# Kernel tuning notes

Measured on AMD Instinct MI355X. Metric: run time of the kernel, lower is better.

## Reference

```python
import jax, jax.numpy as jnp
import numpy as np

M = 2048                      # image side (self.M)
INPUT_SHAPE = (362, 362)      # default forward arg; only used for pad sizing
N_ANGLES = 32
THETA = np.linspace(0.0, np.pi, N_ANGLES)  # radians, as the source uses np.cos(angle)


def _dct_mat(N):
    # DCT-II with norm='ortho': C[k, n] = s_k * cos(pi*(n+0.5)*k/N)
    n = np.arange(N)
    C = np.cos(np.pi * (n[None, :] + 0.5) * n[:, None] / N)
    scale = np.full((N, 1), np.sqrt(2.0 / N))
    scale[0, 0] = np.sqrt(1.0 / N)
    return jnp.asarray((C * scale).astype(np.float32))


def _pad_width():
    diagonal = np.sqrt(2) * max(INPUT_SHAPE)
    pad = [int(np.ceil(diagonal - s)) for s in INPUT_SHAPE]
    new_center = [(s + p) // 2 for s, p in zip(INPUT_SHAPE, pad)]
    old_center = [s // 2 for s in INPUT_SHAPE]
    pad_before = [nc - oc for oc, nc in zip(old_center, new_center)]
    return [(pb, p - pb) for pb, p in zip(pad_before, pad)]


def setup_inputs() -> dict:
    key = jax.random.key(0)
    image = jax.random.normal(key, (M, M), dtype=jnp.float32)
    return {"image": image}


def _forward(image):
    # --- 2D DCT-II (ortho), separable: D = C @ x @ C^T ---
    C = _dct_mat(M)
    d = C @ image @ C.T

    # --- pad (widths derived from input_shape as in the source) ---
    padded = jnp.pad(d, _pad_width())          # [P, P], P = 2198
    P = padded.shape[0]
    center = P // 2

    xs = jnp.arange(P, dtype=jnp.float32)
    yy, xx = jnp.meshgrid(xs, xs, indexing='ij')   # output row (y) / col (x) grid
    angles = jnp.asarray(THETA, dtype=jnp.float32)

    def one_angle(carry, ang):
        cos_a = jnp.cos(ang)
        sin_a = jnp.sin(ang)
        # ImageProjectiveTransformV3 maps output (x, y) -> input coords
        x_in = cos_a * xx + sin_a * yy - center * (cos_a + sin_a - 1.0)
        y_in = -sin_a * xx + cos_a * yy - center * (cos_a - sin_a - 1.0)
        x0 = jnp.floor(x_in)
        y0 = jnp.floor(y_in)
        wx = x_in - x0
        wy = y_in - y0
        # fill_mode='WRAP': wrap sample coordinates modulo image size
        x0i = jnp.mod(x0.astype(jnp.int32), P)
        x1i = (x0i + 1) % P
        y0i = jnp.mod(y0.astype(jnp.int32), P)
        y1i = (y0i + 1) % P
        v00 = padded[y0i, x0i]
        v01 = padded[y0i, x1i]
        v10 = padded[y1i, x0i]
        v11 = padded[y1i, x1i]
        rotated = (1.0 - wy) * ((1.0 - wx) * v00 + wx * v01) \
                + wy * ((1.0 - wx) * v10 + wx * v11)
        # radon line: reduce over rows (axis=0)
        return carry, rotated.sum(axis=0)

    _, lines = jax.lax.scan(one_angle, 0, angles)   # [A, P]
    y = lines.T                                     # [P, A] == tf.transpose(A)
    return y / jnp.max(y)


def reference(image):
    return _forward(image)
```

## Files before the change

kernel.cpp:

```cpp
#include <hip/hip_runtime.h>
#include <hip/hip_bf16.h>
#include <math.h>

#define PDIM 2198
#define PADB 75
#define NANG 32
#define NLINE (NANG * PDIM)

#define CB 32
#define RW 32
#define NWIN 69
#define TS 48
#define TSTRIDE 52

typedef __attribute__((ext_vector_type(8))) short bf16x8;
typedef __attribute__((ext_vector_type(4))) float f32x4;

#define GLOAD_LDS16(g, l)                                              \
    __builtin_amdgcn_global_load_lds(                                  \
        (const __attribute__((address_space(1))) void*)(g),            \
        (__attribute__((address_space(3))) void*)(l), 16, 0, 0)
#define GLOAD_LDS4(g, l)                                               \
    __builtin_amdgcn_global_load_lds(                                  \
        (const __attribute__((address_space(1))) void*)(g),            \
        (__attribute__((address_space(3))) void*)(l), 4, 0, 0)

#if __has_builtin(__builtin_amdgcn_fractf)
#define FRACTF(x) __builtin_amdgcn_fractf(x)
#else
#define FRACTF(x) ((x) - floorf(x))
#endif

__global__ void gen_dct(__hip_bfloat16* __restrict__ C) {
    int idx = blockIdx.x * 256 + threadIdx.x;
    int k = idx >> 11;
    int n = idx & 2047;
    int t = ((2 * n + 1) * k) & 8191;
    float s = sqrtf(((k == 0) ? 1.0f : 2.0f) / 2048.0f);
    C[idx] = __float2bfloat16(s * cospif((float)t * (1.0f / 4096.0f)));
}

__global__ void cvt_img(const float* __restrict__ in, __hip_bfloat16* __restrict__ out) {
    int i = (blockIdx.x * 256 + threadIdx.x) * 4;
    float4 v = *(const float4*)(in + i);
    out[i + 0] = __float2bfloat16(v.x);
    out[i + 1] = __float2bfloat16(v.y);
    out[i + 2] = __float2bfloat16(v.z);
    out[i + 3] = __float2bfloat16(v.w);
}

template<int F32OUT>
__global__ __launch_bounds__(256) void gemm_bt(const __hip_bfloat16* __restrict__ A,
                                               const __hip_bfloat16* __restrict__ B,
                                               void* __restrict__ out,
                                               int ldo, int off) {
    __shared__ __hip_bfloat16 Al[128 * 32];
    __shared__ __hip_bfloat16 Bl[128 * 32];
    const int tid = threadIdx.x;
    const int wid = tid >> 6;
    const int lane = tid & 63;
    const int wr = wid >> 1, wc = wid & 1;
    const int l15 = lane & 15, lhi = lane >> 4;
    const int row0 = blockIdx.y * 128;
    const int col0 = blockIdx.x * 128;

    const __hip_bfloat16* gA = A + (size_t)(row0 + wid * 32 + (lane >> 2)) * 2048 + (lane & 3) * 8;
    const __hip_bfloat16* gB = B + (size_t)(col0 + wid * 32 + (lane >> 2)) * 2048 + (lane & 3) * 8;
    __hip_bfloat16* lA = Al + wid * 1024;
    __hip_bfloat16* lB = Bl + wid * 1024;

    f32x4 acc[4][4] = {};

    for (int k0 = 0; k0 < 2048; k0 += 32) {
        GLOAD_LDS16(gA + k0, lA);
        GLOAD_LDS16(gA + 16 * 2048 + k0, lA + 16 * 32);
        GLOAD_LDS16(gB + k0, lB);
        GLOAD_LDS16(gB + 16 * 2048 + k0, lB + 16 * 32);
        __syncthreads();
        bf16x8 af[4], bfr[4];
#pragma unroll
        for (int m = 0; m < 4; ++m)
            af[m] = *(const bf16x8*)(Al + (wr * 64 + m * 16 + l15) * 32 + lhi * 8);
#pragma unroll
        for (int n = 0; n < 4; ++n)
            bfr[n] = *(const bf16x8*)(Bl + (wc * 64 + n * 16 + l15) * 32 + lhi * 8);
#pragma unroll
        for (int m = 0; m < 4; ++m)
#pragma unroll
            for (int n = 0; n < 4; ++n)
                acc[m][n] = __builtin_amdgcn_mfma_f32_16x16x32_bf16(af[m], bfr[n],
                                                                    acc[m][n], 0, 0, 0);
        __syncthreads();
    }

#pragma unroll
    for (int m = 0; m < 4; ++m) {
        const int row = row0 + wr * 64 + m * 16 + lhi * 4;
#pragma unroll
        for (int n = 0; n < 4; ++n) {
            const int col = col0 + wc * 64 + n * 16 + l15;
            f32x4 v = acc[m][n];
            if (F32OUT) {
                float* p = (float*)out + (size_t)(col + off) * ldo + off + row;
                p[0] = v[0]; p[1] = v[1]; p[2] = v[2]; p[3] = v[3];
            } else {
                __hip_bfloat16* p = (__hip_bfloat16*)out + (size_t)col * 2048 + row;
                p[0] = __float2bfloat16(v[0]);
                p[1] = __float2bfloat16(v[1]);
                p[2] = __float2bfloat16(v[2]);
                p[3] = __float2bfloat16(v[3]);
            }
        }
    }
}

struct AngleArgs {
    float ca[NANG], sa[NANG], ox[NANG], oy[NANG];
};

__global__ __launch_bounds__(256) void radon5(const float* __restrict__ padded,
                                              float* __restrict__ lines,
                                              AngleArgs args) {
    __shared__ float tile[2][TS * TSTRIDE];
    __shared__ float red[4][8];
    const int a = blockIdx.y;
    const int c0 = blockIdx.x * CB;
    const int t = threadIdx.x;
    const int wid = t >> 6, lane = t & 63;
    const int cl = lane >> 3;
    const int rl = lane & 7;
    const int c = c0 + wid * 8 + cl;
    const float ca = args.ca[a], sa = args.sa[a];
    const float ox = args.ox[a], oy = args.oy[a];

    const float cf = (float)c;
    const float xbase = fmaf(ca, cf, ox);
    const float ybase = fmaf(-sa, cf, oy);

    const float xbMin = fminf(fmaf(ca, (float)c0, ox), fmaf(ca, (float)(c0 + CB - 1), ox));
    const float ybMin = fminf(fmaf(-sa, (float)c0, oy), fmaf(-sa, (float)(c0 + CB - 1), oy));
    const bool caPos = (ca >= 0.0f);

    float sum = 0.0f;

    auto origin = [&](int w, int& bx0, int& by0) {
        const float rx = (float)(w * RW);
        const float ry = caPos ? rx : (float)(w * RW + RW - 1);
        bx0 = (int)floorf(fmaf(sa, rx, xbMin)) - 1;
        by0 = (int)floorf(fmaf(ca, ry, ybMin)) - 1;
    };

    auto stage = [&](int buf, int bx0, int by0) {
        int bxs = bx0;
        bxs += (bxs < 0) ? PDIM : 0;
        bxs -= (bxs >= PDIM) ? PDIM : 0;
        if (bxs + TSTRIDE - 1 < PDIM) {
            const int slab = wid * 12;
#pragma unroll
            for (int iss = 0; iss < 3; ++iss) {
                const int d = iss * 256 + lane * 4;
                if (d < 12 * TSTRIDE) {
                    const int rr = d / TSTRIDE;
                    const int col = d - rr * TSTRIDE;
                    int gy = by0 + slab + rr;
                    gy += (gy < 0) ? PDIM : 0;
                    gy -= (gy >= PDIM) ? PDIM : 0;
                    GLOAD_LDS16(padded + (size_t)gy * PDIM + bxs + col,
                                &tile[buf][slab * TSTRIDE + iss * 256]);
                }
            }
        } else {
            if (lane < TSTRIDE) {
                int gx = bx0 + lane;
                gx += (gx < 0) ? PDIM : 0;
                gx -= (gx >= PDIM) ? PDIM : 0;
#pragma unroll
                for (int j = 0; j < 12; ++j) {
                    const int row = wid * 12 + j;
                    int gy = by0 + row;
                    gy += (gy < 0) ? PDIM : 0;
                    gy -= (gy >= PDIM) ? PDIM : 0;
                    GLOAD_LDS4(padded + (size_t)gy * PDIM + gx,
                               &tile[buf][row * TSTRIDE]);
                }
            }
        }
    };

    auto compute = [&](int r0, int buf, int bx0, int by0, bool last) {
        const float bx0f = (float)bx0, by0f = (float)by0;
        const float* tb = &tile[buf][0];
#pragma unroll
        for (int k = 0; k < 4; ++k) {
            const int r = r0 + rl + 8 * k;
            const float rf = (float)r;
            const float x_in = fmaf(sa, rf, xbase);
            const float y_in = fmaf(ca, rf, ybase);
            const float xl = x_in - bx0f;
            const float yl = y_in - by0f;
            const int xi = (int)xl;
            const int yi = (int)yl;
            const float wx = FRACTF(xl);
            const float wy = FRACTF(yl);
            const float* p = tb + yi * TSTRIDE + xi;
            const float v00 = p[0], v01 = p[1];
            const float v10 = p[TSTRIDE], v11 = p[TSTRIDE + 1];
            const float top = fmaf(wx, v01 - v00, v00);
            const float bot = fmaf(wx, v11 - v10, v10);
            if (!last || r < PDIM) sum = fmaf(wy, bot - top, sum + top);
        }
    };

    int bxc, byc, bxn, byn;
    origin(0, bxc, byc);
    stage(0, bxc, byc);
    __syncthreads();
    for (int w = 0; w < NWIN - 1; ++w) {
        origin(w + 1, bxn, byn);
        stage((w + 1) & 1, bxn, byn);
        compute(w * RW, w & 1, bxc, byc, false);
        __syncthreads();
        bxc = bxn; byc = byn;
    }
    compute((NWIN - 1) * RW, (NWIN - 1) & 1, bxc, byc, true);

    sum += __shfl_xor(sum, 1, 64);
    sum += __shfl_xor(sum, 2, 64);
    sum += __shfl_xor(sum, 4, 64);
    if (rl == 0) red[wid][cl] = sum;
    __syncthreads();
    if (t < 32 && c0 + t < PDIM)
        lines[a * PDIM + c0 + t] = red[t >> 3][t & 7];
}

__global__ __launch_bounds__(256) void max_k(const float* __restrict__ lines,
                                             unsigned int* __restrict__ gmax) {
    const int idx = blockIdx.x * 256 + threadIdx.x;
    float m = (idx < NLINE) ? lines[idx] : -3.4e38f;
#pragma unroll
    for (int off = 32; off > 0; off >>= 1)
        m = fmaxf(m, __shfl_down(m, off, 64));
    __shared__ float wm[4];
    const int lane = threadIdx.x & 63, wid = threadIdx.x >> 6;
    if (lane == 0) wm[wid] = m;
    __syncthreads();
    if (threadIdx.x == 0) {
        float bm = fmaxf(fmaxf(wm[0], wm[1]), fmaxf(wm[2], wm[3]));
        unsigned int b = __float_as_uint(bm);
        unsigned int key = (b & 0x80000000u) ? ~b : (b | 0x80000000u);
        atomicMax(gmax, key);
    }
}

__global__ void norm_k(const float* __restrict__ lines,
                       const unsigned int* __restrict__ gmax,
                       float* __restrict__ out) {
    int idx = blockIdx.x * 256 + threadIdx.x;
    if (idx >= NLINE) return;
    unsigned int u = *gmax;
    unsigned int b = (u & 0x80000000u) ? (u & 0x7fffffffu) : ~u;
    float mx = __uint_as_float(b);
    int c = idx >> 5;
    int a = idx & 31;
    out[idx] = lines[(size_t)a * PDIM + c] / mx;
}

extern "C" void kernel_launch(void* const* d_in, const int* in_sizes, int n_in,
                              void* d_out, int out_size, void* d_ws, size_t ws_size,
                              hipStream_t stream) {
    (void)in_sizes; (void)n_in; (void)out_size; (void)ws_size;
    const float* img = (const float*)d_in[0];
    float* out = (float*)d_out;

    __hip_bfloat16* Cbf   = (__hip_bfloat16*)d_ws;
    __hip_bfloat16* imgbf = Cbf + 4194304;
    __hip_bfloat16* uT    = imgbf + 4194304;
    float* padded  = (float*)(uT + 4194304);
    float* lines   = padded + (size_t)PDIM * PDIM;
    unsigned int* gmax = (unsigned int*)(lines + NLINE);

    hipMemsetAsync(padded, 0, (size_t)PDIM * PDIM * sizeof(float), stream);
    hipMemsetAsync(gmax, 0, sizeof(unsigned int), stream);

    gen_dct<<<16384, 256, 0, stream>>>(Cbf);
    cvt_img<<<4096, 256, 0, stream>>>(img, imgbf);

    dim3 gg(16, 16);
    gemm_bt<0><<<gg, 256, 0, stream>>>(imgbf, Cbf, uT, 2048, 0);
    gemm_bt<1><<<gg, 256, 0, stream>>>(uT, Cbf, padded, PDIM, PADB);

    AngleArgs aa;
    for (int i = 0; i < NANG; ++i) {
        float th = (float)((double)i * 3.14159265358979323846 / 31.0);
        float ca = (float)cos((double)th);
        float sa = (float)sin((double)th);
        aa.ca[i] = ca;
        aa.sa[i] = sa;
        aa.ox[i] = -1099.0f * (ca + sa - 1.0f);
        aa.oy[i] = -1099.0f * (ca - sa - 1.0f);
    }
    radon5<<<dim3(NWIN, NANG), 256, 0, stream>>>(padded, lines, aa);
    max_k<<<(NLINE + 255) / 256, 256, 0, stream>>>(lines, gmax);
    norm_k<<<(NLINE + 255) / 256, 256, 0, stream>>>(lines, gmax, out);
}
```

Measured before the change: 352.8 us.

## Deepen radon prefetch to four buffers, pad row stride, narrow GEMM tiles

The radon kernel now keeps four LDS tile buffers and prefetches two windows ahead. It uses explicit vmcnt waits and a single raw barrier per window instead of double buffering with two __syncthreads. Padded rows get a 2252-float stride so the zeroed columns past the edge stand in for the wrapped columns. That removes the slow per-element 4-byte wrap load path and always uses 16-byte global-to-LDS loads. The GEMM tile shrinks from 128x128 to 128x64, doubling the block count for better CU occupancy at the cost of less operand reuse.

```diff
diff --git a/kernel.cpp b/kernel.cpp
--- a/kernel.cpp
+++ b/kernel.cpp
@@ -3,6 +3,7 @@
 #include <math.h>
 
 #define PDIM 2198
+#define PDIM2 2252
 #define PADB 75
 #define NANG 32
 #define NLINE (NANG * PDIM)
@@ -12,6 +13,7 @@
 #define NWIN 69
 #define TS 48
 #define TSTRIDE 52
+#define NBUF 4
 
 typedef __attribute__((ext_vector_type(8))) short bf16x8;
 typedef __attribute__((ext_vector_type(4))) float f32x4;
@@ -20,10 +22,6 @@
     __builtin_amdgcn_global_load_lds(                                  \
         (const __attribute__((address_space(1))) void*)(g),            \
         (__attribute__((address_space(3))) void*)(l), 16, 0, 0)
-#define GLOAD_LDS4(g, l)                                               \
-    __builtin_amdgcn_global_load_lds(                                  \
-        (const __attribute__((address_space(1))) void*)(g),            \
-        (__attribute__((address_space(3))) void*)(l), 4, 0, 0)
 
 #if __has_builtin(__builtin_amdgcn_fractf)
 #define FRACTF(x) __builtin_amdgcn_fractf(x)
@@ -55,39 +53,38 @@
                                                void* __restrict__ out,
                                                int ldo, int off) {
     __shared__ __hip_bfloat16 Al[128 * 32];
-    __shared__ __hip_bfloat16 Bl[128 * 32];
+    __shared__ __hip_bfloat16 Bl[64 * 32];
     const int tid = threadIdx.x;
     const int wid = tid >> 6;
     const int lane = tid & 63;
     const int wr = wid >> 1, wc = wid & 1;
     const int l15 = lane & 15, lhi = lane >> 4;
     const int row0 = blockIdx.y * 128;
-    const int col0 = blockIdx.x * 128;
+    const int col0 = blockIdx.x * 64;
 
     const __hip_bfloat16* gA = A + (size_t)(row0 + wid * 32 + (lane >> 2)) * 2048 + (lane & 3) * 8;
-    const __hip_bfloat16* gB = B + (size_t)(col0 + wid * 32 + (lane >> 2)) * 2048 + (lane & 3) * 8;
+    const __hip_bfloat16* gB = B + (size_t)(col0 + wid * 16 + (lane >> 2)) * 2048 + (lane & 3) * 8;
     __hip_bfloat16* lA = Al + wid * 1024;
-    __hip_bfloat16* lB = Bl + wid * 1024;
-
-    f32x4 acc[4][4] = {};
+    __hip_bfloat16* lB = Bl + wid * 512;
+
+    f32x4 acc[4][2] = {};
 
     for (int k0 = 0; k0 < 2048; k0 += 32) {
         GLOAD_LDS16(gA + k0, lA);
         GLOAD_LDS16(gA + 16 * 2048 + k0, lA + 16 * 32);
         GLOAD_LDS16(gB + k0, lB);
-        GLOAD_LDS16(gB + 16 * 2048 + k0, lB + 16 * 32);
         __syncthreads();
-        bf16x8 af[4], bfr[4];
+        bf16x8 af[4], bfr[2];
 #pragma unroll
         for (int m = 0; m < 4; ++m)
             af[m] = *(const bf16x8*)(Al + (wr * 64 + m * 16 + l15) * 32 + lhi * 8);
 #pragma unroll
-        for (int n = 0; n < 4; ++n)
-            bfr[n] = *(const bf16x8*)(Bl + (wc * 64 + n * 16 + l15) * 32 + lhi * 8);
+        for (int n = 0; n < 2; ++n)
+            bfr[n] = *(const bf16x8*)(Bl + (wc * 32 + n * 16 + l15) * 32 + lhi * 8);
 #pragma unroll
         for (int m = 0; m < 4; ++m)
 #pragma unroll
-            for (int n = 0; n < 4; ++n)
+            for (int n = 0; n < 2; ++n)
                 acc[m][n] = __builtin_amdgcn_mfma_f32_16x16x32_bf16(af[m], bfr[n],
                                                                     acc[m][n], 0, 0, 0);
         __syncthreads();
@@ -97,8 +94,8 @@
     for (int m = 0; m < 4; ++m) {
         const int row = row0 + wr * 64 + m * 16 + lhi * 4;
 #pragma unroll
-        for (int n = 0; n < 4; ++n) {
-            const int col = col0 + wc * 64 + n * 16 + l15;
+        for (int n = 0; n < 2; ++n) {
+            const int col = col0 + wc * 32 + n * 16 + l15;
             f32x4 v = acc[m][n];
             if (F32OUT) {
                 float* p = (float*)out + (size_t)(col + off) * ldo + off + row;
@@ -118,10 +115,10 @@
     float ca[NANG], sa[NANG], ox[NANG], oy[NANG];
 };
 
-__global__ __launch_bounds__(256) void radon5(const float* __restrict__ padded,
+__global__ __launch_bounds__(256) void radon6(const float* __restrict__ padded,
                                               float* __restrict__ lines,
                                               AngleArgs args) {
-    __shared__ float tile[2][TS * TSTRIDE];
+    __shared__ float tile[NBUF][TS * TSTRIDE];
     __shared__ float red[4][8];
     const int a = blockIdx.y;
     const int c0 = blockIdx.x * CB;
@@ -154,50 +151,32 @@
         int bxs = bx0;
         bxs += (bxs < 0) ? PDIM : 0;
         bxs -= (bxs >= PDIM) ? PDIM : 0;
-        if (bxs + TSTRIDE - 1 < PDIM) {
-            const int slab = wid * 12;
-#pragma unroll
-            for (int iss = 0; iss < 3; ++iss) {
-                const int d = iss * 256 + lane * 4;
-                if (d < 12 * TSTRIDE) {
-                    const int rr = d / TSTRIDE;
-                    const int col = d - rr * TSTRIDE;
-                    int gy = by0 + slab + rr;
-                    gy += (gy < 0) ? PDIM : 0;
-                    gy -= (gy >= PDIM) ? PDIM : 0;
-                    GLOAD_LDS16(padded + (size_t)gy * PDIM + bxs + col,
-                                &tile[buf][slab * TSTRIDE + iss * 256]);
-                }
+        const int slab = wid * 12;
+#pragma unroll
+        for (int iss = 0; iss < 3; ++iss) {
+            const int d = iss * 256 + lane * 4;
+            if (d < 12 * TSTRIDE) {
+                const int rr = d / TSTRIDE;
+                const int col = d - rr * TSTRIDE;
+                int gy = by0 + slab + rr;
+                gy += (gy < 0) ? PDIM : 0;
+                gy -= (gy >= PDIM) ? PDIM : 0;
+                GLOAD_LDS16(padded + (size_t)gy * PDIM2 + bxs + col,
+                            &tile[buf][slab * TSTRIDE + iss * 256]);
             }
-        } else {
-            if (lane < TSTRIDE) {
-                int gx = bx0 + lane;
-                gx += (gx < 0) ? PDIM : 0;
-                gx -= (gx >= PDIM) ? PDIM : 0;
-#pragma unroll
-                for (int j = 0; j < 12; ++j) {
-                    const int row = wid * 12 + j;
-                    int gy = by0 + row;
-                    gy += (gy < 0) ? PDIM : 0;
-                    gy -= (gy >= PDIM) ? PDIM : 0;
-                    GLOAD_LDS4(padded + (size_t)gy * PDIM + gx,
-                               &tile[buf][row * TSTRIDE]);
-                }
-            }
         }
     };
 
     auto compute = [&](int r0, int buf, int bx0, int by0, bool last) {
-        const float bx0f = (float)bx0, by0f = (float)by0;
+        const float xbb = xbase - (float)bx0;
+        const float ybb = ybase - (float)by0;
         const float* tb = &tile[buf][0];
 #pragma unroll
         for (int k = 0; k < 4; ++k) {
             const int r = r0 + rl + 8 * k;
             const float rf = (float)r;
-            const float x_in = fmaf(sa, rf, xbase);
-            const float y_in = fmaf(ca, rf, ybase);
-            const float xl = x_in - bx0f;
-            const float yl = y_in - by0f;
+            const float xl = fmaf(sa, rf, xbb);
+            const float yl = fmaf(ca, rf, ybb);
             const int xi = (int)xl;
             const int yi = (int)yl;
             const float wx = FRACTF(xl);
@@ -211,18 +190,25 @@
         }
     };
 
-    int bxc, byc, bxn, byn;
-    origin(0, bxc, byc);
-    stage(0, bxc, byc);
-    __syncthreads();
-    for (int w = 0; w < NWIN - 1; ++w) {
-        origin(w + 1, bxn, byn);
-        stage((w + 1) & 1, bxn, byn);
-        compute(w * RW, w & 1, bxc, byc, false);
-        __syncthreads();
-        bxc = bxn; byc = byn;
-    }
-    compute((NWIN - 1) * RW, (NWIN - 1) & 1, bxc, byc, true);
+    int bx[NWIN > 0 ? 4 : 4], by[4];
+    origin(0, bx[0], by[0]);
+    stage(0, bx[0], by[0]);
+    origin(1, bx[1], by[1]);
+    stage(1, bx[1], by[1]);
+    for (int w = 0; w < NWIN; ++w) {
+        if (w + 2 < NWIN) {
+            int bxn, byn;
+            origin(w + 2, bxn, byn);
+            bx[(w + 2) & 3] = bxn; by[(w + 2) & 3] = byn;
+            stage((w + 2) & 3, bxn, byn);
+        }
+        if (w < NWIN - 2)       asm volatile("s_waitcnt vmcnt(6)" ::: "memory");
+        else if (w == NWIN - 2) asm volatile("s_waitcnt vmcnt(3)" ::: "memory");
+        else                    asm volatile("s_waitcnt vmcnt(0)" ::: "memory");
+        __builtin_amdgcn_s_barrier();
+        __builtin_amdgcn_sched_barrier(0);
+        compute(w * RW, w & 3, bx[w & 3], by[w & 3], w == NWIN - 1);
+    }
 
     sum += __shfl_xor(sum, 1, 64);
     sum += __shfl_xor(sum, 2, 64);
@@ -276,18 +262,17 @@
     __hip_bfloat16* imgbf = Cbf + 4194304;
     __hip_bfloat16* uT    = imgbf + 4194304;
     float* padded  = (float*)(uT + 4194304);
-    float* lines   = padded + (size_t)PDIM * PDIM;
+    float* lines   = padded + (size_t)PDIM * PDIM2;
     unsigned int* gmax = (unsigned int*)(lines + NLINE);
 
-    hipMemsetAsync(padded, 0, (size_t)PDIM * PDIM * sizeof(float), stream);
+    hipMemsetAsync(padded, 0, (size_t)PDIM * PDIM2 * sizeof(float), stream);
     hipMemsetAsync(gmax, 0, sizeof(unsigned int), stream);
 
     gen_dct<<<16384, 256, 0, stream>>>(Cbf);
     cvt_img<<<4096, 256, 0, stream>>>(img, imgbf);
 
-    dim3 gg(16, 16);
-    gemm_bt<0><<<gg, 256, 0, stream>>>(imgbf, Cbf, uT, 2048, 0);
-    gemm_bt<1><<<gg, 256, 0, stream>>>(uT, Cbf, padded, PDIM, PADB);
+    gemm_bt<0><<<dim3(32, 16), 256, 0, stream>>>(imgbf, Cbf, uT, 2048, 0);
+    gemm_bt<1><<<dim3(32, 16), 256, 0, stream>>>(uT, Cbf, padded, PDIM2, PADB);
 
     AngleArgs aa;
     for (int i = 0; i < NANG; ++i) {
@@ -299,7 +284,7 @@
         aa.ox[i] = -1099.0f * (ca + sa - 1.0f);
         aa.oy[i] = -1099.0f * (ca - sa - 1.0f);
     }
-    radon5<<<dim3(NWIN, NANG), 256, 0, stream>>>(padded, lines, aa);
+    radon6<<<dim3(NWIN, NANG), 256, 0, stream>>>(padded, lines, aa);
     max_k<<<(NLINE + 255) / 256, 256, 0, stream>>>(lines, gmax);
     norm_k<<<(NLINE + 255) / 256, 256, 0, stream>>>(lines, gmax, out);
 }
```

New measurement: 318.8 us. 1.11x faster.
